# Performance work log

Hardware: AMD Instinct MI355X
Metric: run time of the kernel (lower is better)

Reference implementation:

```python
import jax, jax.numpy as jnp
import numpy as np

# Config constants (mirror cfg)
B, N, C = 2, 6, 64
H_IMG, W_IMG = 256, 704
DS = 16
DSH, DSW = H_IMG // DS, W_IMG // DS      # 16, 44
D0, D1 = 4, 45                            # depth bins -> D = 41
X, Y, Z = 200, 200, 1                     # bev_dim


def _make_frustum():
    d = jnp.arange(D0, D1, dtype=jnp.float32)            # (D,)
    D = d.shape[0]
    xg = jnp.linspace(0.0, W_IMG - 1.0, DSW, dtype=jnp.float32)
    yg = jnp.linspace(0.0, H_IMG - 1.0, DSH, dtype=jnp.float32)
    depth = jnp.broadcast_to(d[:, None, None], (D, DSH, DSW))
    xx = jnp.broadcast_to(xg[None, None, :], (D, DSH, DSW))
    yy = jnp.broadcast_to(yg[None, :, None], (D, DSH, DSW))
    return jnp.stack([xx, yy, depth], axis=-1)            # (D, dsH, dsW, 3)


def setup_inputs() -> dict:
    key = jax.random.key(0)
    k1, k2, k3 = jax.random.split(key, 3)
    D = D1 - D0
    image_feature = jax.random.normal(k1, (B, N, D, DSH, DSW, C), dtype=jnp.float32)
    post_trans = 0.1 * jax.random.normal(k2, (B, N, 3), dtype=jnp.float32)
    post_rots = jnp.broadcast_to(jnp.eye(3, dtype=jnp.float32), (B, N, 3, 3))
    K = jnp.array([[500.0, 0.0, W_IMG / 2.0],
                   [0.0, 500.0, H_IMG / 2.0],
                   [0.0, 0.0, 1.0]], dtype=jnp.float32)
    intrinsics = jnp.broadcast_to(K, (B, N, 3, 3))
    tr = jax.random.normal(k3, (B, N, 3), dtype=jnp.float32)
    extrinsics = jnp.tile(jnp.eye(4, dtype=jnp.float32), (B, N, 1, 1)).at[..., :3, 3].set(tr)
    frustum = _make_frustum()
    bev_res = jnp.array([0.5, 0.5, 100.0], dtype=jnp.float32)       # [res_x, res_y, z_hi - z_lo]
    bev_start_pos = jnp.array([-50.0, -50.0, 0.0], dtype=jnp.float32)
    return {
        "image_feature": image_feature,
        "post_trans": post_trans,
        "post_rots": post_rots,
        "intrinsics": intrinsics,
        "extrinsics": extrinsics,
        "frustum": frustum,
        "bev_res": bev_res,
        "bev_start_pos": bev_start_pos,
    }


def _get_geometry(frustum, post_trans, post_rots, intrinsics, extrinsics):
    ext_inv = jnp.linalg.inv(extrinsics)                    # (B,N,4,4)
    rot = ext_inv[..., :3, :3]
    trans = ext_inv[..., :3, 3]
    # undo image-space augmentation
    pts = frustum[None, None] - post_trans[:, :, None, None, None, :]   # (B,N,D,h,w,3)
    pts = jnp.einsum('bnij,bndhwj->bndhwi', jnp.linalg.inv(post_rots), pts)
    # (u*d, v*d, d)
    pts = jnp.concatenate([pts[..., :2] * pts[..., 2:3], pts[..., 2:3]], axis=-1)
    comb = rot @ jnp.linalg.inv(intrinsics)                 # (B,N,3,3)
    pts = jnp.einsum('bnij,bndhwj->bndhwi', comb, pts)
    return pts + trans[:, :, None, None, None, :]


def reference(image_feature, post_trans, post_rots, intrinsics, extrinsics,
              frustum, bev_res, bev_start_pos):
    Bc, Nc, D, dsH, dsW, Cc = image_feature.shape
    geom = _get_geometry(frustum, post_trans, post_rots, intrinsics, extrinsics)
    Np = Nc * D * dsH * dsW
    feats = image_feature.reshape(Bc, Np, Cc)
    coords = (geom - (bev_start_pos - bev_res / 2.0)) / bev_res
    # torch .long() truncates toward zero; int cast in jax does the same
    ci = jax.lax.stop_gradient(coords).reshape(Bc, Np, 3).astype(jnp.int32)
    mask = ((ci[..., 0] >= 0) & (ci[..., 0] < X) &
            (ci[..., 1] >= 0) & (ci[..., 1] < Y) &
            (ci[..., 2] >= 0) & (ci[..., 2] < Z))
    rank = ci[..., 0] * (Y * Z) + ci[..., 1] * Z + ci[..., 2]
    rank = jnp.where(mask, rank, X * Y * Z)                 # dummy overflow bucket
    f = jnp.where(mask[..., None], feats, jnp.zeros((), feats.dtype))
    # sort + cumsum-trick segment sum + scatter == one segment_sum into the flat grid
    pool = jax.vmap(lambda r, x: jax.ops.segment_sum(x, r, num_segments=X * Y * Z + 1))(rank, f)
    bev = pool[:, :X * Y * Z].reshape(Bc, X, Y, Z, Cc)[:, :, :, 0]   # Z == 1
    return jnp.transpose(bev, (0, 3, 1, 2))                 # (B, C, X, Y)
```

## Files before the change

kernel.cpp:

```cpp
#include <hip/hip_runtime.h>
#include <hip/hip_fp16.h>

#define B_ 2
#define N_ 6
#define D_ 41
#define H_ 16
#define W_ 44
#define C_ 64
#define X_ 200
#define Y_ 200
#define NPTS (B_*N_*D_*H_*W_)
#define NBN (B_*N_)
#define NCELL (B_*X_*Y_)
#define MAT_STRIDE 24
#define KREP 4
#define STAGE_F4 ((size_t)KREP*NCELL*32*8/16)

__device__ inline void pk_add_f16(__half2* addr, __half2 val) {
    unsigned int u = *reinterpret_cast<unsigned int*>(&val);
    asm volatile("global_atomic_pk_add_f16 %0, %1, off"
                 :: "v"((unsigned long long)(uintptr_t)addr), "v"(u)
                 : "memory");
}

__device__ inline void inv3x3(const double m[9], double out[9]) {
    double a=m[0],b=m[1],c=m[2],d=m[3],e=m[4],f=m[5],g=m[6],h=m[7],i=m[8];
    double A  =  (e*i - f*h);
    double Bm = -(d*i - f*g);
    double Cm =  (d*h - e*g);
    double det = a*A + b*Bm + c*Cm;
    double id = 1.0/det;
    out[0] = A*id;   out[1] = -(b*i - c*h)*id; out[2] =  (b*f - c*e)*id;
    out[3] = Bm*id;  out[4] =  (a*i - c*g)*id; out[5] = -(a*f - c*d)*id;
    out[6] = Cm*id;  out[7] = -(a*h - b*g)*id; out[8] =  (a*e - b*d)*id;
}

__global__ void prep_kernel(const float* __restrict__ post_rots,
                            const float* __restrict__ intr,
                            const float* __restrict__ extr,
                            double* __restrict__ mats) {
    int bn = threadIdx.x;
    if (bn >= NBN) return;

    double pr[9], prinv[9], kk[9], kin[9];
    for (int i=0;i<9;i++) pr[i] = (double)post_rots[bn*9+i];
    inv3x3(pr, prinv);
    for (int i=0;i<9;i++) kk[i] = (double)intr[bn*9+i];
    inv3x3(kk, kin);

    const float* E = extr + bn*16;
    double a00=E[0], a01=E[1], a02=E[2], a03=E[3];
    double a10=E[4], a11=E[5], a12=E[6], a13=E[7];
    double a20=E[8], a21=E[9], a22=E[10], a23=E[11];
    double a30=E[12], a31=E[13], a32=E[14], a33=E[15];

    double s0=a00*a11-a10*a01, s1=a00*a12-a10*a02, s2=a00*a13-a10*a03;
    double s3=a01*a12-a11*a02, s4=a01*a13-a11*a03, s5=a02*a13-a12*a03;
    double c5=a22*a33-a32*a23, c4=a21*a33-a31*a23, c3=a21*a32-a31*a22;
    double c2=a20*a33-a30*a23, c1=a20*a32-a30*a22, c0=a20*a31-a30*a21;
    double det = s0*c5 - s1*c4 + s2*c3 + s3*c2 - s4*c1 + s5*c0;
    double iv = 1.0/det;

    double rot[9], trans[3];
    rot[0] = ( a11*c5 - a12*c4 + a13*c3)*iv;
    rot[1] = (-a01*c5 + a02*c4 - a03*c3)*iv;
    rot[2] = ( a31*s5 - a32*s4 + a33*s3)*iv;
    trans[0]=(-a21*s5 + a22*s4 - a23*s3)*iv;
    rot[3] = (-a10*c5 + a12*c2 - a13*c1)*iv;
    rot[4] = ( a00*c5 - a02*c2 + a03*c1)*iv;
    rot[5] = (-a30*s5 + a32*s2 - a33*s1)*iv;
    trans[1]=( a20*s5 - a22*s2 + a23*s1)*iv;
    rot[6] = ( a10*c4 - a11*c2 + a13*c0)*iv;
    rot[7] = (-a00*c4 + a01*c2 - a03*c0)*iv;
    rot[8] = ( a30*s4 - a31*s2 + a33*s0)*iv;
    trans[2]=(-a20*s4 + a21*s2 - a23*s0)*iv;

    double comb[9];
    for (int i=0;i<3;i++) for (int j=0;j<3;j++)
        comb[i*3+j] = rot[i*3+0]*kin[0+j] + rot[i*3+1]*kin[3+j] + rot[i*3+2]*kin[6+j];

    double* o = mats + (size_t)bn*MAT_STRIDE;
    for (int i=0;i<9;i++) o[i]   = prinv[i];
    for (int i=0;i<9;i++) o[9+i] = comb[i];
    for (int i=0;i<3;i++) o[18+i]= trans[i];
}

__global__ __launch_bounds__(256)
void geom_kernel(const float* __restrict__ post_trans,
                 const float* __restrict__ frustum,
                 const float* __restrict__ bev_res,
                 const float* __restrict__ bev_start,
                 const double* __restrict__ mats,
                 int* __restrict__ rank,
                 float4* __restrict__ stage4) {
    int p = blockIdx.x * blockDim.x + threadIdx.x;

    const float4 z4 = make_float4(0.f, 0.f, 0.f, 0.f);
    for (size_t i = (size_t)p; i < STAGE_F4; i += (size_t)NPTS)
        stage4[i] = z4;

    if (p >= NPTS) return;

    int w = p % W_; int t = p / W_;
    int h = t % H_;  t /= H_;
    int d = t % D_;  t /= D_;
    int bn = t;      int b = bn / N_;

    const double* M = mats + (size_t)bn*MAT_STRIDE;
    int fidx = ((d*H_ + h)*W_ + w)*3;
    double fx = (double)frustum[fidx+0];
    double fy = (double)frustum[fidx+1];
    double fz = (double)frustum[fidx+2];

    double px = fx - (double)post_trans[bn*3+0];
    double py = fy - (double)post_trans[bn*3+1];
    double pz = fz - (double)post_trans[bn*3+2];

    double q0 = M[0]*px + M[1]*py + M[2]*pz;
    double q1 = M[3]*px + M[4]*py + M[5]*pz;
    double q2 = M[6]*px + M[7]*py + M[8]*pz;

    double r0 = q0*q2, r1 = q1*q2, r2 = q2;

    double gx = M[9]*r0  + M[10]*r1 + M[11]*r2 + M[18];
    double gy = M[12]*r0 + M[13]*r1 + M[14]*r2 + M[19];
    double gz = M[15]*r0 + M[16]*r1 + M[17]*r2 + M[20];

    double resx = (double)bev_res[0], resy = (double)bev_res[1], resz = (double)bev_res[2];
    double sx = (double)bev_start[0] - resx*0.5;
    double sy = (double)bev_start[1] - resy*0.5;
    double sz = (double)bev_start[2] - resz*0.5;

    int cx = (int)((gx - sx)/resx);
    int cy = (int)((gy - sy)/resy);
    int cz = (int)((gz - sz)/resz);

    int cell = -1;
    if (cx >= 0 && cx < X_ && cy >= 0 && cy < Y_ && cz == 0)
        cell = (b*X_ + cx)*Y_ + cy;
    rank[p] = cell;
}

__global__ __launch_bounds__(256)
void scatter_2x4(const float2* __restrict__ feat2,
                 const int* __restrict__ rank,
                 __half2* __restrict__ stage) {
    int tid  = blockIdx.x * blockDim.x + threadIdx.x;
    int q    = tid >> 6;
    int lane = tid & 63;
    int half = lane >> 5;
    int k    = lane & 31;

    int s  = q / 88;
    int r  = q % 88;
    int hp = r / 11;
    int wb = r % 11;
    int pbase = s*(H_*W_) + (hp*2 + half)*W_ + wb*4;

    __half2* rep = stage + (size_t)(q & (KREP-1)) * ((size_t)NCELL*32);

    int runCell = -1;
    float rx = 0.f, ry = 0.f;
    #pragma unroll
    for (int i = 0; i < 4; ++i) {
        int p = pbase + i;
        int c = rank[p];
        float vx = 0.f, vy = 0.f;
        if (c >= 0) { float2 v = feat2[(size_t)p*32 + k]; vx = v.x; vy = v.y; }

        int   oc = __shfl_xor(c, 32);
        float ox = __shfl_xor(vx, 32);
        float oy = __shfl_xor(vy, 32);
        if (c >= 0 && c == oc) {
            if (half == 0) { vx += ox; vy += oy; }
            else c = -1;
        }

        if (c >= 0) {
            if (c == runCell) { rx += vx; ry += vy; }
            else {
                if (runCell >= 0) {
                    __half2 hv; hv.x = __float2half(rx); hv.y = __float2half(ry);
                    pk_add_f16(&rep[(size_t)runCell*32 + k], hv);
                }
                runCell = c; rx = vx; ry = vy;
            }
        }
    }
    if (runCell >= 0) {
        __half2 hv; hv.x = __float2half(rx); hv.y = __float2half(ry);
        pk_add_f16(&rep[(size_t)runCell*32 + k], hv);
    }
}

__global__ __launch_bounds__(512)
void trans_h2(const __half2* __restrict__ stage, float* __restrict__ out) {
    __shared__ float tile[64][65];
    int b   = blockIdx.y;
    int xy0 = blockIdx.x * 64;
    int tx  = threadIdx.x & 31;
    int ty  = threadIdx.x >> 5;

    const size_t rstride = (size_t)NCELL*32;
    #pragma unroll
    for (int i = 0; i < 4; ++i) {
        int r = ty + i*16;
        size_t idx = ((size_t)b*(X_*Y_) + xy0 + r)*32 + tx;
        float sx = 0.f, sy = 0.f;
        #pragma unroll
        for (int kk = 0; kk < KREP; ++kk) {
            float2 f = __half22float2(stage[kk*rstride + idx]);
            sx += f.x; sy += f.y;
        }
        tile[r][2*tx]   = sx;
        tile[r][2*tx+1] = sy;
    }
    __syncthreads();
    int cw = threadIdx.x >> 6;
    int j  = threadIdx.x & 63;
    #pragma unroll
    for (int k = 0; k < 8; ++k) {
        int c = cw*8 + k;
        out[((size_t)(b*C_ + c))*(X_*Y_) + xy0 + j] = tile[j][c];
    }
}

__global__ __launch_bounds__(256)
void geom_only(const float* __restrict__ post_trans,
               const float* __restrict__ frustum,
               const float* __restrict__ bev_res,
               const float* __restrict__ bev_start,
               const double* __restrict__ mats,
               int* __restrict__ rank) {
    int p = blockIdx.x * blockDim.x + threadIdx.x;
    if (p >= NPTS) return;
    int w = p % W_; int t = p / W_;
    int h = t % H_;  t /= H_;
    int d = t % D_;  t /= D_;
    int bn = t;      int b = bn / N_;
    const double* M = mats + (size_t)bn*MAT_STRIDE;
    int fidx = ((d*H_ + h)*W_ + w)*3;
    double fx = (double)frustum[fidx+0];
    double fy = (double)frustum[fidx+1];
    double fz = (double)frustum[fidx+2];
    double px = fx - (double)post_trans[bn*3+0];
    double py = fy - (double)post_trans[bn*3+1];
    double pz = fz - (double)post_trans[bn*3+2];
    double q0 = M[0]*px + M[1]*py + M[2]*pz;
    double q1 = M[3]*px + M[4]*py + M[5]*pz;
    double q2 = M[6]*px + M[7]*py + M[8]*pz;
    double r0 = q0*q2, r1 = q1*q2, r2 = q2;
    double gx = M[9]*r0  + M[10]*r1 + M[11]*r2 + M[18];
    double gy = M[12]*r0 + M[13]*r1 + M[14]*r2 + M[19];
    double gz = M[15]*r0 + M[16]*r1 + M[17]*r2 + M[20];
    double resx = (double)bev_res[0], resy = (double)bev_res[1], resz = (double)bev_res[2];
    double sx = (double)bev_start[0] - resx*0.5;
    double sy = (double)bev_start[1] - resy*0.5;
    double sz = (double)bev_start[2] - resz*0.5;
    int cx = (int)((gx - sx)/resx);
    int cy = (int)((gy - sy)/resy);
    int cz = (int)((gz - sz)/resz);
    int cell = -1;
    if (cx >= 0 && cx < X_ && cy >= 0 && cy < Y_ && cz == 0)
        cell = (b*X_ + cx)*Y_ + cy;
    rank[p] = cell;
}

__global__ __launch_bounds__(256)
void scatter_fallback(const float* __restrict__ feat,
                      const int* __restrict__ rank,
                      float* __restrict__ dst) {
    int tid  = blockIdx.x * blockDim.x + threadIdx.x;
    int p    = tid >> 6;
    int lane = tid & 63;
    if (p >= NPTS) return;
    int cell = rank[p];
    if (cell < 0) return;
    int b = cell / (X_*Y_);
    int xy = cell % (X_*Y_);
    float v = feat[(size_t)p*C_ + lane];
    unsafeAtomicAdd(&dst[((size_t)(b*C_ + lane))*(X_*Y_) + xy], v);
}

extern "C" void kernel_launch(void* const* d_in, const int* in_sizes, int n_in,
                              void* d_out, int out_size, void* d_ws, size_t ws_size,
                              hipStream_t stream) {
    const float* feat       = (const float*)d_in[0];
    const float* post_trans = (const float*)d_in[1];
    const float* post_rots  = (const float*)d_in[2];
    const float* intr       = (const float*)d_in[3];
    const float* extr       = (const float*)d_in[4];
    const float* frustum    = (const float*)d_in[5];
    const float* bev_res    = (const float*)d_in[6];
    const float* bev_start  = (const float*)d_in[7];
    float* out = (float*)d_out;

    char* base = (char*)d_ws;
    double* mats   = (double*)base;                    size_t off = 4096;
    int* rank      = (int*)(base + off);               off += (size_t)NPTS*4;
    off = (off + 511) & ~(size_t)511;
    __half2* stage = (__half2*)(base + off);
    const size_t stage_bytes = (size_t)KREP * NCELL * C_ * 2;
    off += stage_bytes;
    bool have_ws = (ws_size >= off);

    hipLaunchKernelGGL(prep_kernel, dim3(1), dim3(16), 0, stream,
                       post_rots, intr, extr, mats);

    const int pt_blocks = (NPTS + 255) / 256;

    if (have_ws) {
        geom_kernel<<<pt_blocks, 256, 0, stream>>>(post_trans, frustum, bev_res,
                                                   bev_start, mats, rank,
                                                   (float4*)stage);
        const int sc_blocks = (int)(((size_t)(NPTS/8)*64 + 255) / 256);
        scatter_2x4<<<sc_blocks, 256, 0, stream>>>((const float2*)feat, rank, stage);
        trans_h2<<<dim3((X_*Y_)/64, B_), 512, 0, stream>>>(stage, out);
    } else {
        hipMemsetAsync(out, 0, (size_t)out_size*sizeof(float), stream);
        geom_only<<<pt_blocks, 256, 0, stream>>>(post_trans, frustum, bev_res,
                                                 bev_start, mats, rank);
        const int wv_blocks = (int)(((size_t)NPTS*64 + 255) / 256);
        scatter_fallback<<<wv_blocks, 256, 0, stream>>>(feat, rank, out);
    }
}
```

Before: 75.51 us.

## Scatter by walking depth runs per pixel column with prefetched loads

```diff
diff --git a/kernel.cpp b/kernel.cpp
--- a/kernel.cpp
+++ b/kernel.cpp
@@ -15,12 +15,12 @@
 #define MAT_STRIDE 24
 #define KREP 4
 #define STAGE_F4 ((size_t)KREP*NCELL*32*8/16)
-
-__device__ inline void pk_add_f16(__half2* addr, __half2 val) {
+#define NWAVE_SC (NBN*H_*(W_/2))
+
+__device__ inline void pk_add_f16_nc(__half2* addr, __half2 val) {
     unsigned int u = *reinterpret_cast<unsigned int*>(&val);
     asm volatile("global_atomic_pk_add_f16 %0, %1, off"
-                 :: "v"((unsigned long long)(uintptr_t)addr), "v"(u)
-                 : "memory");
+                 :: "v"((unsigned long long)(uintptr_t)addr), "v"(u));
 }
 
 __device__ inline void inv3x3(const double m[9], double out[9]) {
@@ -142,54 +142,57 @@
 }
 
 __global__ __launch_bounds__(256)
-void scatter_2x4(const float2* __restrict__ feat2,
-                 const int* __restrict__ rank,
-                 __half2* __restrict__ stage) {
+void scatter_druns(const float2* __restrict__ feat2,
+                   const int* __restrict__ rank,
+                   __half2* __restrict__ stage) {
     int tid  = blockIdx.x * blockDim.x + threadIdx.x;
     int q    = tid >> 6;
     int lane = tid & 63;
     int half = lane >> 5;
     int k    = lane & 31;
-
-    int s  = q / 88;
-    int r  = q % 88;
-    int hp = r / 11;
-    int wb = r % 11;
-    int pbase = s*(H_*W_) + (hp*2 + half)*W_ + wb*4;
+    if (q >= NWAVE_SC) return;
+
+    int wp = q % (W_/2);
+    int t  = q / (W_/2);
+    int h  = t % H_;
+    int bn = t / H_;
+    int w  = wp*2 + half;
 
     __half2* rep = stage + (size_t)(q & (KREP-1)) * ((size_t)NCELL*32);
+
+    const int pstride = H_*W_;
+    int p = (bn*D_*H_ + h)*W_ + w;
+
+    int   c = rank[p];
+    float2 v = feat2[(size_t)p*32 + k];
 
     int runCell = -1;
     float rx = 0.f, ry = 0.f;
-    #pragma unroll
-    for (int i = 0; i < 4; ++i) {
-        int p = pbase + i;
-        int c = rank[p];
-        float vx = 0.f, vy = 0.f;
-        if (c >= 0) { float2 v = feat2[(size_t)p*32 + k]; vx = v.x; vy = v.y; }
-
-        int   oc = __shfl_xor(c, 32);
-        float ox = __shfl_xor(vx, 32);
-        float oy = __shfl_xor(vy, 32);
-        if (c >= 0 && c == oc) {
-            if (half == 0) { vx += ox; vy += oy; }
-            else c = -1;
+
+    for (int d = 0; d < D_; ++d) {
+        int   cn = -1;
+        float2 vn = make_float2(0.f, 0.f);
+        if (d + 1 < D_) {
+            int pn = p + pstride;
+            cn = rank[pn];
+            vn = feat2[(size_t)pn*32 + k];
+            p = pn;
         }
-
         if (c >= 0) {
-            if (c == runCell) { rx += vx; ry += vy; }
+            if (c == runCell) { rx += v.x; ry += v.y; }
             else {
                 if (runCell >= 0) {
                     __half2 hv; hv.x = __float2half(rx); hv.y = __float2half(ry);
-                    pk_add_f16(&rep[(size_t)runCell*32 + k], hv);
+                    pk_add_f16_nc(&rep[(size_t)runCell*32 + k], hv);
                 }
-                runCell = c; rx = vx; ry = vy;
+                runCell = c; rx = v.x; ry = v.y;
             }
         }
+        c = cn; v = vn;
     }
     if (runCell >= 0) {
         __half2 hv; hv.x = __float2half(rx); hv.y = __float2half(ry);
-        pk_add_f16(&rep[(size_t)runCell*32 + k], hv);
+        pk_add_f16_nc(&rep[(size_t)runCell*32 + k], hv);
     }
 }
 
@@ -313,8 +316,8 @@
         geom_kernel<<<pt_blocks, 256, 0, stream>>>(post_trans, frustum, bev_res,
                                                    bev_start, mats, rank,
                                                    (float4*)stage);
-        const int sc_blocks = (int)(((size_t)(NPTS/8)*64 + 255) / 256);
-        scatter_2x4<<<sc_blocks, 256, 0, stream>>>((const float2*)feat, rank, stage);
+        const int sc_blocks = (NWAVE_SC * 64) / 256;
+        scatter_druns<<<sc_blocks, 256, 0, stream>>>((const float2*)feat, rank, stage);
         trans_h2<<<dim3((X_*Y_)/64, B_), 512, 0, stream>>>(stage, out);
     } else {
         hipMemsetAsync(out, 0, (size_t)out_size*sizeof(float), stream);
```

Measured after the change: 74.55 us. About the same (-1.3%).
